# Optimization experiments

Hardware: AMD Instinct MI355X
Metric: run time of the kernel (lower is better)

The kernel has to match this reference:

```python
import jax, jax.numpy as jnp
import numpy as np

B, L, D, H = 8, 1024, 1024, 16
DPH = D // H  # 64


def setup_inputs() -> dict:
    key = jax.random.key(0)
    ks = jax.random.split(key, 12)
    s = 1.0 / np.sqrt(D)
    return {
        "key": jax.random.normal(ks[0], (B, L, D), jnp.float32),
        "value": jax.random.normal(ks[1], (B, L, D), jnp.float32),
        "query": jax.random.normal(ks[2], (B, L, D), jnp.float32),
        "attn_mask": jax.random.randint(ks[3], (B, L, L), 0, 2) > 0,
        "Wq": jax.random.normal(ks[4], (D, D), jnp.float32) * s,
        "bq": jnp.zeros((D,), jnp.float32),
        "Wk": jax.random.normal(ks[5], (D, D), jnp.float32) * s,
        "bk": jnp.zeros((D,), jnp.float32),
        "Wv": jax.random.normal(ks[6], (D, D), jnp.float32) * s,
        "bv": jnp.zeros((D,), jnp.float32),
        "Wo": jax.random.normal(ks[7], (D, D), jnp.float32) * s,
        "bo": jnp.zeros((D,), jnp.float32),
        "gamma": jnp.ones((D,), jnp.float32),
        "beta": jnp.zeros((D,), jnp.float32),
    }


def _layer_norm(x, gamma, beta, eps=1e-5):
    mu = jnp.mean(x, axis=-1, keepdims=True)
    var = jnp.var(x, axis=-1, keepdims=True)
    return (x - mu) * jax.lax.rsqrt(var + eps) * gamma + beta


def reference(key, value, query, attn_mask, Wq, bq, Wk, bk, Wv, bv, Wo, bo, gamma, beta):
    residual = query
    k = key @ Wk + bk      # [B, L, D]
    v = value @ Wv + bv
    q = query @ Wq + bq
    # faithful to torch: raw row-major view into [B*H, L, dph] (NOT standard head transpose)
    k = k.reshape(B * H, -1, DPH)
    v = v.reshape(B * H, -1, DPH)
    q = q.reshape(B * H, -1, DPH)
    # faithful to torch repeat: tile whole batch H times along dim 0
    mask = jnp.tile(attn_mask, (H, 1, 1))  # [B*H, L, L]
    scale = DPH ** (-0.5)
    scores = jnp.einsum('bqd,bkd->bqk', q, k) * scale
    scores = jnp.where(mask, jnp.float32(-1e9), scores)
    attention = jax.nn.softmax(scores, axis=2)
    context = jnp.einsum('bqk,bkd->bqd', attention, v)  # [B*H, L, dph]
    context = context.reshape(B, -1, D)
    output = context @ Wo + bo
    output = _layer_norm(residual + output, gamma, beta)
    return (output, attention)
```

## Files before the change

kernel.cpp:

```cpp
#include <hip/hip_runtime.h>

typedef __attribute__((ext_vector_type(8))) short short8;
typedef __attribute__((ext_vector_type(4))) float f32x4;

#define AS1C(p) ((const __attribute__((address_space(1))) void*)(p))
#define AS3(p)  ((__attribute__((address_space(3))) void*)(p))

__device__ __forceinline__ unsigned short f2bf(float f) {
  unsigned int u = __float_as_uint(f);
  return (unsigned short)((u + 0x7fffu + ((u >> 16) & 1u)) >> 16);
}

__device__ __forceinline__ void gload16(const void* g, void* l) {
  __builtin_amdgcn_global_load_lds(AS1C(g), AS3(l), 16, 0, 0);
}

#define EXP_C 0.18033688011112042f

__global__ __launch_bounds__(256) void conv3_bf16(const float* __restrict__ s0,
                                                  const float* __restrict__ s1,
                                                  const float* __restrict__ s2,
                                                  unsigned short* __restrict__ d0,
                                                  unsigned short* __restrict__ d1,
                                                  unsigned short* __restrict__ d2, int n4) {
  const float* in = (blockIdx.z == 0) ? s0 : (blockIdx.z == 1) ? s1 : s2;
  unsigned short* out = (blockIdx.z == 0) ? d0 : (blockIdx.z == 1) ? d1 : d2;
  int i = blockIdx.x * 256 + threadIdx.x;
  if (i >= n4) return;
  float4 v = ((const float4*)in)[i];
  ushort4 o;
  o.x = f2bf(v.x); o.y = f2bf(v.y); o.z = f2bf(v.z); o.w = f2bf(v.w);
  ((ushort4*)out)[i] = o;
}

__global__ __launch_bounds__(256) void prep_kernel(const float* __restrict__ W0,
                                                   const float* __restrict__ W1,
                                                   const float* __restrict__ W2,
                                                   const float* __restrict__ W3,
                                                   unsigned short* __restrict__ WtBase,
                                                   const int* __restrict__ m,
                                                   unsigned int* __restrict__ bitsT) {
  int bid = blockIdx.x;
  if (bid < 4096) {
    __shared__ float t[32][33];
    int z = bid >> 10;
    int rb = bid & 1023;
    int bx = (rb & 31) * 32, by = (rb >> 5) * 32;
    const float* W = (z == 0) ? W0 : (z == 1) ? W1 : (z == 2) ? W2 : W3;
    unsigned short* Wt = WtBase + (size_t)z * 1024 * 1024;
    int tx = threadIdx.x & 31, ty = threadIdx.x >> 5;
#pragma unroll
    for (int i = 0; i < 4; ++i) {
      int r = ty + i * 8;
      t[r][tx] = W[(size_t)(by + r) * 1024 + bx + tx];
    }
    __syncthreads();
#pragma unroll
    for (int i = 0; i < 4; ++i) {
      int r = ty + i * 8;
      Wt[(size_t)(bx + r) * 1024 + by + tx] = f2bf(t[tx][r]);
    }
  } else {
    int i = (bid - 4096) * 256 + threadIdx.x;
    unsigned long long bl = __ballot(m[i] != 0);
    if ((threadIdx.x & 63) == 0) {
      int b_ = i >> 20, q = (i >> 10) & 1023, k = i & 1023;
      int w = k >> 5;
      bitsT[b_ * 32768 + w * 1024 + q]       = (unsigned int)bl;
      bitsT[b_ * 32768 + (w + 1) * 1024 + q] = (unsigned int)(bl >> 32);
    }
  }
}

__global__ __launch_bounds__(256) void transpose_v(const unsigned short* __restrict__ v,
                                                   unsigned short* __restrict__ vt) {
  __shared__ unsigned short t[32][33];
  int b = blockIdx.z;
  int bx = blockIdx.x * 32;
  int by = blockIdx.y * 32;
  int tx = threadIdx.x & 31, ty = threadIdx.x >> 5;
#pragma unroll
  for (int i = 0; i < 4; ++i) {
    int r = ty + i * 8;
    t[r][tx] = v[(size_t)b * 65536 + (size_t)(by + r) * 64 + bx + tx];
  }
  __syncthreads();
#pragma unroll
  for (int i = 0; i < 4; ++i) {
    int r = ty + i * 8;
    vt[(size_t)b * 65536 + (size_t)(bx + r) * 1024 + by + tx] = t[tx][r];
  }
}

template <int MODE>
__device__ __forceinline__ void gemm_body(
    const unsigned short* __restrict__ A, const unsigned short* __restrict__ Bt,
    const float* __restrict__ bias, const float* __restrict__ res,
    unsigned short* __restrict__ Cb, float* __restrict__ Cf,
    unsigned short* lA, unsigned short* lB) {
  const int K = 1024, N = 1024;
  const int tid = threadIdx.x;
  const int wave = tid >> 6, lane = tid & 63;
  const int row_l = lane & 15, kg = lane >> 4;
  const int wg = blockIdx.y * 8 + blockIdx.x;
  const int idx = (wg & 7) * 64 + (wg >> 3);
  const int m0 = (idx >> 3) * 128, n0 = (idx & 7) * 128;
  const int wm = (wave >> 1) * 64, wn = (wave & 1) * 64;
  f32x4 acc[4][4] = {};

  for (int k0 = 0; k0 < K; k0 += 32) {
    __syncthreads();
#pragma unroll
    for (int it = 0; it < 2; ++it) {
      int c = wave * 64 + it * 256 + lane;
      int r = c >> 2, ch = c & 3;
      int sch = ch ^ (r & 3);
      gload16(A + (size_t)(m0 + r) * K + k0 + sch * 8, lA + (wave * 64 + it * 256) * 8);
      gload16(Bt + (size_t)(n0 + r) * K + k0 + sch * 8, lB + (wave * 64 + it * 256) * 8);
    }
    __syncthreads();
    short8 af[4], bfr[4];
#pragma unroll
    for (int t = 0; t < 4; ++t) {
      int ra = wm + t * 16 + row_l;
      af[t] = *(const short8*)(lA + ra * 32 + ((kg ^ (ra & 3)) << 3));
      int rb = wn + t * 16 + row_l;
      bfr[t] = *(const short8*)(lB + rb * 32 + ((kg ^ (rb & 3)) << 3));
    }
    __builtin_amdgcn_s_setprio(1);
#pragma unroll
    for (int mt = 0; mt < 4; ++mt)
#pragma unroll
      for (int nt = 0; nt < 4; ++nt)
        acc[mt][nt] = __builtin_amdgcn_mfma_f32_16x16x32_bf16(af[mt], bfr[nt], acc[mt][nt], 0, 0, 0);
    __builtin_amdgcn_s_setprio(0);
  }
#pragma unroll
  for (int mt = 0; mt < 4; ++mt)
#pragma unroll
    for (int nt = 0; nt < 4; ++nt)
#pragma unroll
      for (int r = 0; r < 4; ++r) {
        int grow = m0 + wm + mt * 16 + kg * 4 + r;
        int gcol = n0 + wn + nt * 16 + row_l;
        float v = acc[mt][nt][r] + bias[gcol];
        if (MODE == 0) {
          Cb[(size_t)grow * N + gcol] = f2bf(v);
        } else {
          v += res[(size_t)grow * N + gcol];
          Cf[(size_t)grow * N + gcol] = v;
        }
      }
}

__global__ __launch_bounds__(256) void gemm_qkv_kernel(
    const unsigned short* __restrict__ A0, const unsigned short* __restrict__ A1,
    const unsigned short* __restrict__ A2, const unsigned short* __restrict__ WtBase,
    const float* __restrict__ b0, const float* __restrict__ b1, const float* __restrict__ b2,
    unsigned short* __restrict__ C0, unsigned short* __restrict__ C1,
    unsigned short* __restrict__ C2) {
  __shared__ unsigned short lA[128 * 32];
  __shared__ unsigned short lB[128 * 32];
  int z = blockIdx.z;
  const unsigned short* A = (z == 0) ? A0 : (z == 1) ? A1 : A2;
  const float* bias = (z == 0) ? b0 : (z == 1) ? b1 : b2;
  unsigned short* C = (z == 0) ? C0 : (z == 1) ? C1 : C2;
  gemm_body<0>(A, WtBase + (size_t)z * 1024 * 1024, bias, nullptr, C, nullptr, lA, lB);
}

__global__ __launch_bounds__(256) void gemm_out_kernel(
    const unsigned short* __restrict__ A, const unsigned short* __restrict__ Bt,
    const float* __restrict__ bias, const float* __restrict__ res, float* __restrict__ Cf) {
  __shared__ unsigned short lA[128 * 32];
  __shared__ unsigned short lB[128 * 32];
  gemm_body<1>(A, Bt, bias, res, nullptr, Cf, lA, lB);
}

__global__ __launch_bounds__(256) void attn_kernel(
    const unsigned short* __restrict__ Q,
    const unsigned short* __restrict__ Km,
    const unsigned short* __restrict__ Vt,
    const unsigned int* __restrict__ mbitsT,
    float* __restrict__ attn,
    unsigned short* __restrict__ ctx) {
  __shared__ unsigned short lQ[64 * 64];
  __shared__ unsigned short lK[64 * 64];
  __shared__ unsigned short lV[64 * 64];
  const int tid = threadIdx.x, wave = tid >> 6, lane = tid & 63;
  const int row_l = lane & 15, kg = lane >> 4;
  const int wg = blockIdx.y * 16 + blockIdx.x;
  const int idx = (wg & 7) * 256 + (wg >> 3);
  const int batch = idx >> 4, qt = idx & 15;
  const int q0 = qt * 64;
  const unsigned short* Qb = Q + (size_t)batch * 65536;
  const unsigned short* Kb = Km + (size_t)batch * 65536;
  const unsigned short* Vb = Vt + (size_t)batch * 65536;
  const unsigned int* mT = mbitsT + (size_t)(batch & 7) * 32768;
  float* attb = attn + (size_t)batch * 1048576;
  const int q_loc = wave * 16 + row_l;
  const int q_lane = q0 + q_loc;

#define STAGE_K_TO(kt, dst)                                                           \
  {                                                                                   \
    _Pragma("unroll") for (int it = 0; it < 2; ++it) {                                \
      int c = wave * 64 + it * 256 + lane;                                            \
      int r_ = c >> 3, ch_ = c & 7, sch_ = ch_ ^ (r_ & 7);                            \
      gload16(Kb + (size_t)((kt) * 64 + r_) * 64 + sch_ * 8,                          \
              (dst) + (wave * 64 + it * 256) * 8);                                    \
    }                                                                                 \
  }
#define STAGE_V_TO(kt, dst)                                                           \
  {                                                                                   \
    _Pragma("unroll") for (int it = 0; it < 2; ++it) {                                \
      int c = wave * 64 + it * 256 + lane;                                            \
      int r_ = c >> 3, ch_ = c & 7, sch_ = ch_ ^ (r_ & 7);                            \
      gload16(Vb + (size_t)r_ * 1024 + (kt) * 64 + sch_ * 8,                          \
              (dst) + (wave * 64 + it * 256) * 8);                                    \
    }                                                                                 \
  }
#define WAIT_BAR0                                             \
  asm volatile("s_waitcnt vmcnt(0)" ::: "memory");            \
  __builtin_amdgcn_s_barrier();

#pragma unroll
  for (int it = 0; it < 2; ++it) {
    int c = wave * 64 + it * 256 + lane;
    int r = c >> 3, ch = c & 7;
    int sch = ch ^ (r & 7);
    gload16(Qb + (size_t)(q0 + r) * 64 + sch * 8, lQ + (wave * 64 + it * 256) * 8);
  }
  STAGE_K_TO(0, lK)
  WAIT_BAR0
  short8 qf[2];
#pragma unroll
  for (int kk = 0; kk < 2; ++kk)
    qf[kk] = *(const short8*)(lQ + q_loc * 64 + (((kk * 4 + kg) ^ (q_loc & 7)) << 3));

  float l_part = 0.f;

  auto pass1_step = [&](const unsigned short* kbuf, int kt) {
    unsigned int mw0 = mT[(kt * 2 + 0) * 1024 + q_lane];
    unsigned int mw1 = mT[(kt * 2 + 1) * 1024 + q_lane];
    f32x4 s[4];
    __builtin_amdgcn_s_setprio(1);
#pragma unroll
    for (int cf = 0; cf < 4; ++cf) {
      int rk = cf * 16 + row_l;
      f32x4 a = {0.f, 0.f, 0.f, 0.f};
#pragma unroll
      for (int kk = 0; kk < 2; ++kk) {
        short8 kf = *(const short8*)(kbuf + rk * 64 + (((kk * 4 + kg) ^ (rk & 7)) << 3));
        a = __builtin_amdgcn_mfma_f32_16x16x32_bf16(kf, qf[kk], a, 0, 0, 0);
      }
      s[cf] = a;
    }
    __builtin_amdgcn_s_setprio(0);
#pragma unroll
    for (int cf = 0; cf < 4; ++cf) {
      unsigned int w = (cf < 2) ? mw0 : mw1;
#pragma unroll
      for (int r = 0; r < 4; ++r) {
        int bit = (w >> ((cf & 1) * 16 + kg * 4 + r)) & 1;
        float e = __builtin_exp2f(s[cf][r] * EXP_C);
        l_part += bit ? 0.f : e;
      }
    }
  };
  for (int kt2 = 0; kt2 < 16; kt2 += 2) {
    STAGE_K_TO(kt2 + 1, lV)
    pass1_step(lK, kt2);
    WAIT_BAR0
    if (kt2 + 2 < 16) STAGE_K_TO(kt2 + 2, lK)
    pass1_step(lV, kt2 + 1);
    WAIT_BAR0
  }
  float se = l_part;
  se += __shfl_xor(se, 16);
  se += __shfl_xor(se, 32);
  const float il = 1.f / se;

  f32x4 cacc[4] = {};
  unsigned short* lP = lQ;

  for (int kt = 0; kt < 16; ++kt) {
    __syncthreads();
    STAGE_K_TO(kt, lK)
    STAGE_V_TO(kt, lV)
    WAIT_BAR0
    unsigned int mw0 = mT[(kt * 2 + 0) * 1024 + q_lane];
    unsigned int mw1 = mT[(kt * 2 + 1) * 1024 + q_lane];
    f32x4 s[4];
    __builtin_amdgcn_s_setprio(1);
#pragma unroll
    for (int cf = 0; cf < 4; ++cf) {
      int rk = cf * 16 + row_l;
      f32x4 a = {0.f, 0.f, 0.f, 0.f};
#pragma unroll
      for (int kk = 0; kk < 2; ++kk) {
        short8 kf = *(const short8*)(lK + rk * 64 + (((kk * 4 + kg) ^ (rk & 7)) << 3));
        a = __builtin_amdgcn_mfma_f32_16x16x32_bf16(kf, qf[kk], a, 0, 0, 0);
      }
      s[cf] = a;
    }
    __builtin_amdgcn_s_setprio(0);
#pragma unroll
    for (int cf = 0; cf < 4; ++cf) {
      unsigned int w = (cf < 2) ? mw0 : mw1;
      f32x4 o;
      unsigned short pb[4];
#pragma unroll
      for (int r = 0; r < 4; ++r) {
        int bit = (w >> ((cf & 1) * 16 + kg * 4 + r)) & 1;
        float p = bit ? 0.f : __builtin_exp2f(s[cf][r] * EXP_C) * il;
        o[r] = p;
        pb[r] = f2bf(p);
      }
      int swc = (cf * 2 + (kg >> 1)) ^ (q_loc & 7);
      *(uint2*)((char*)lP + q_loc * 128 + swc * 16 + (kg & 1) * 8) = *(const uint2*)pb;
      __builtin_nontemporal_store(
          o, (f32x4*)(attb + (size_t)q_lane * 1024 + kt * 64 + cf * 16 + kg * 4));
    }
    __builtin_amdgcn_s_setprio(1);
#pragma unroll
    for (int kk = 0; kk < 2; ++kk) {
      short8 pa = *(const short8*)(lP + q_loc * 64 + (((kk * 4 + kg) ^ (q_loc & 7)) << 3));
#pragma unroll
      for (int df = 0; df < 4; ++df) {
        int rv = df * 16 + row_l;
        short8 vb = *(const short8*)(lV + rv * 64 + (((kk * 4 + kg) ^ (rv & 7)) << 3));
        cacc[df] = __builtin_amdgcn_mfma_f32_16x16x32_bf16(pa, vb, cacc[df], 0, 0, 0);
      }
    }
    __builtin_amdgcn_s_setprio(0);
  }
#pragma unroll
  for (int df = 0; df < 4; ++df)
#pragma unroll
    for (int r = 0; r < 4; ++r) {
      int grow = q0 + wave * 16 + kg * 4 + r;
      int gcol = df * 16 + row_l;
      ctx[(size_t)batch * 65536 + (size_t)grow * 64 + gcol] = f2bf(cacc[df][r]);
    }
#undef STAGE_K_TO
#undef STAGE_V_TO
#undef WAIT_BAR0
}

__global__ __launch_bounds__(256) void layernorm_kernel(float* __restrict__ io,
                                                        const float* __restrict__ gamma,
                                                        const float* __restrict__ beta) {
  int wave = threadIdx.x >> 6, lane = threadIdx.x & 63;
  size_t row = (size_t)blockIdx.x * 4 + wave;
  float* p = io + row * 1024;
  float4 v[4];
  float s = 0.f, ss = 0.f;
#pragma unroll
  for (int i = 0; i < 4; ++i) {
    v[i] = ((const float4*)p)[lane + i * 64];
    s += v[i].x + v[i].y + v[i].z + v[i].w;
    ss += v[i].x * v[i].x + v[i].y * v[i].y + v[i].z * v[i].z + v[i].w * v[i].w;
  }
#pragma unroll
  for (int m = 1; m < 64; m <<= 1) { s += __shfl_xor(s, m); ss += __shfl_xor(ss, m); }
  float mu = s * (1.f / 1024.f);
  float var = ss * (1.f / 1024.f) - mu * mu;
  float rinv = rsqrtf(var + 1e-5f);
#pragma unroll
  for (int i = 0; i < 4; ++i) {
    int idx = lane + i * 64;
    float4 g = ((const float4*)gamma)[idx];
    float4 b = ((const float4*)beta)[idx];
    float4 o;
    o.x = (v[i].x - mu) * rinv * g.x + b.x;
    o.y = (v[i].y - mu) * rinv * g.y + b.y;
    o.z = (v[i].z - mu) * rinv * g.z + b.z;
    o.w = (v[i].w - mu) * rinv * g.w + b.w;
    ((float4*)p)[idx] = o;
  }
}

extern "C" void kernel_launch(void* const* d_in, const int* in_sizes, int n_in,
                              void* d_out, int out_size, void* d_ws, size_t ws_size,
                              hipStream_t stream) {
  const float* key   = (const float*)d_in[0];
  const float* value = (const float*)d_in[1];
  const float* query = (const float*)d_in[2];
  const int* amask   = (const int*)d_in[3];
  const float* Wq = (const float*)d_in[4];
  const float* bq = (const float*)d_in[5];
  const float* Wk = (const float*)d_in[6];
  const float* bk = (const float*)d_in[7];
  const float* Wv = (const float*)d_in[8];
  const float* bv = (const float*)d_in[9];
  const float* Wo = (const float*)d_in[10];
  const float* bo = (const float*)d_in[11];
  const float* gamma = (const float*)d_in[12];
  const float* beta  = (const float*)d_in[13];

  char* ws = (char*)d_ws;
  const size_t MB = 1024 * 1024;
  float* out_f = (float*)d_out;
  float* attn_f = (float*)d_out + (size_t)8388608;
  const int n4 = 8388608 / 4;
  dim3 gemm_grid(8, 64);
  dim3 gemm_grid3(8, 64, 3);
  dim3 attn_grid(16, 128);

  const bool big_ws = ws_size >= 106 * MB;
  if (big_ws) {
    unsigned short* A0 = (unsigned short*)(ws + 0);
    unsigned short* A1 = (unsigned short*)(ws + 16 * MB);
    unsigned short* A2 = (unsigned short*)(ws + 32 * MB);
    unsigned short* B1 = (unsigned short*)(ws + 48 * MB);
    unsigned short* B2 = (unsigned short*)(ws + 64 * MB);
    unsigned short* B3 = (unsigned short*)(ws + 80 * MB);
    unsigned short* Wts = (unsigned short*)(ws + 96 * MB);
    unsigned int* mbitsT = (unsigned int*)(ws + 104 * MB);

    prep_kernel<<<36864, 256, 0, stream>>>(Wq, Wk, Wv, Wo, Wts, amask, mbitsT);
    conv3_bf16<<<dim3(8192, 1, 3), 256, 0, stream>>>(query, key, value, A0, A1, A2, n4);
    gemm_qkv_kernel<<<gemm_grid3, 256, 0, stream>>>(A0, A1, A2, Wts, bq, bk, bv, B1, B2, B3);
    transpose_v<<<dim3(2, 32, 128), 256, 0, stream>>>(B3, A1);
    attn_kernel<<<attn_grid, 256, 0, stream>>>(B1, B2, A1, mbitsT, attn_f, A2);
    gemm_out_kernel<<<gemm_grid, 256, 0, stream>>>(A2, Wts + 3 * MB, bo, query, out_f);
    layernorm_kernel<<<2048, 256, 0, stream>>>(out_f, gamma, beta);
  } else {
    unsigned short* B0 = (unsigned short*)(ws + 0);
    unsigned short* B1 = (unsigned short*)(ws + 16 * MB);
    unsigned short* B2 = (unsigned short*)(ws + 32 * MB);
    unsigned short* B3 = (unsigned short*)(ws + 48 * MB);
    unsigned short* Wts = (unsigned short*)(ws + 64 * MB);
    unsigned int* mbitsT = (unsigned int*)(ws + 72 * MB);

    prep_kernel<<<36864, 256, 0, stream>>>(Wq, Wk, Wv, Wo, Wts, amask, mbitsT);
    conv3_bf16<<<dim3(8192, 1, 1), 256, 0, stream>>>(query, query, query, B0, B0, B0, n4);
    gemm_qkv_kernel<<<gemm_grid, 256, 0, stream>>>(B0, B0, B0, Wts, bq, bq, bq, B1, B1, B1);
    conv3_bf16<<<dim3(8192, 1, 1), 256, 0, stream>>>(key, key, key, B0, B0, B0, n4);
    gemm_qkv_kernel<<<gemm_grid, 256, 0, stream>>>(B0, B0, B0, Wts + 1 * MB, bk, bk, bk, B2, B2, B2);
    conv3_bf16<<<dim3(8192, 1, 1), 256, 0, stream>>>(value, value, value, B0, B0, B0, n4);
    gemm_qkv_kernel<<<gemm_grid, 256, 0, stream>>>(B0, B0, B0, Wts + 2 * MB, bv, bv, bv, B3, B3, B3);
    transpose_v<<<dim3(2, 32, 128), 256, 0, stream>>>(B3, B0);
    attn_kernel<<<attn_grid, 256, 0, stream>>>(B1, B2, B0, mbitsT, attn_f, B3);
    gemm_out_kernel<<<gemm_grid, 256, 0, stream>>>(B3, Wts + 3 * MB, bo, query, out_f);
    layernorm_kernel<<<2048, 256, 0, stream>>>(out_f, gamma, beta);
  }
}
```

Before: 344.0 us.

## Double GEMM K-tile to 64 and fold input bf16 conversion into prep kernel

The GEMM mainloop now stages a 64-wide K slice per iteration instead of 32, using an 8-way XOR swizzle, and runs two MFMA sub-steps per barrier pair. This halves the number of synchronisation rounds and global-to-LDS load phases. LDS use per block doubles to 32 KB, which may lower occupancy. Separately, the fp32-to-bf16 conversion of query/key/value is merged into prep_kernel as extra blocks, saving one kernel launch on the large-workspace path.

After: 321.6 us. 6.5% less time.

```diff
diff --git a/kernel.cpp b/kernel.cpp
--- a/kernel.cpp
+++ b/kernel.cpp
@@ -16,22 +16,6 @@
 }
 
 #define EXP_C 0.18033688011112042f
-
-__global__ __launch_bounds__(256) void conv3_bf16(const float* __restrict__ s0,
-                                                  const float* __restrict__ s1,
-                                                  const float* __restrict__ s2,
-                                                  unsigned short* __restrict__ d0,
-                                                  unsigned short* __restrict__ d1,
-                                                  unsigned short* __restrict__ d2, int n4) {
-  const float* in = (blockIdx.z == 0) ? s0 : (blockIdx.z == 1) ? s1 : s2;
-  unsigned short* out = (blockIdx.z == 0) ? d0 : (blockIdx.z == 1) ? d1 : d2;
-  int i = blockIdx.x * 256 + threadIdx.x;
-  if (i >= n4) return;
-  float4 v = ((const float4*)in)[i];
-  ushort4 o;
-  o.x = f2bf(v.x); o.y = f2bf(v.y); o.z = f2bf(v.z); o.w = f2bf(v.w);
-  ((ushort4*)out)[i] = o;
-}
 
 __global__ __launch_bounds__(256) void prep_kernel(const float* __restrict__ W0,
                                                    const float* __restrict__ W1,
@@ -39,7 +23,13 @@
                                                    const float* __restrict__ W3,
                                                    unsigned short* __restrict__ WtBase,
                                                    const int* __restrict__ m,
-                                                   unsigned int* __restrict__ bitsT) {
+                                                   unsigned int* __restrict__ bitsT,
+                                                   const float* __restrict__ s0,
+                                                   const float* __restrict__ s1,
+                                                   const float* __restrict__ s2,
+                                                   unsigned short* __restrict__ d0,
+                                                   unsigned short* __restrict__ d1,
+                                                   unsigned short* __restrict__ d2) {
   int bid = blockIdx.x;
   if (bid < 4096) {
     __shared__ float t[32][33];
@@ -60,7 +50,7 @@
       int r = ty + i * 8;
       Wt[(size_t)(bx + r) * 1024 + by + tx] = f2bf(t[tx][r]);
     }
-  } else {
+  } else if (bid < 36864) {
     int i = (bid - 4096) * 256 + threadIdx.x;
     unsigned long long bl = __ballot(m[i] != 0);
     if ((threadIdx.x & 63) == 0) {
@@ -69,7 +59,27 @@
       bitsT[b_ * 32768 + w * 1024 + q]       = (unsigned int)bl;
       bitsT[b_ * 32768 + (w + 1) * 1024 + q] = (unsigned int)(bl >> 32);
     }
-  }
+  } else {
+    int cb = bid - 36864;
+    int z = cb >> 13;
+    const float* in = (z == 0) ? s0 : (z == 1) ? s1 : s2;
+    unsigned short* out = (z == 0) ? d0 : (z == 1) ? d1 : d2;
+    int i = (cb & 8191) * 256 + threadIdx.x;
+    float4 v = ((const float4*)in)[i];
+    ushort4 o;
+    o.x = f2bf(v.x); o.y = f2bf(v.y); o.z = f2bf(v.z); o.w = f2bf(v.w);
+    ((ushort4*)out)[i] = o;
+  }
+}
+
+__global__ __launch_bounds__(256) void conv_bf16(const float* __restrict__ in,
+                                                 unsigned short* __restrict__ out, int n4) {
+  int i = blockIdx.x * 256 + threadIdx.x;
+  if (i >= n4) return;
+  float4 v = ((const float4*)in)[i];
+  ushort4 o;
+  o.x = f2bf(v.x); o.y = f2bf(v.y); o.z = f2bf(v.z); o.w = f2bf(v.w);
+  ((ushort4*)out)[i] = o;
 }
 
 __global__ __launch_bounds__(256) void transpose_v(const unsigned short* __restrict__ v,
@@ -108,32 +118,35 @@
   const int wm = (wave >> 1) * 64, wn = (wave & 1) * 64;
   f32x4 acc[4][4] = {};
 
-  for (int k0 = 0; k0 < K; k0 += 32) {
+  for (int k0 = 0; k0 < K; k0 += 64) {
     __syncthreads();
 #pragma unroll
-    for (int it = 0; it < 2; ++it) {
+    for (int it = 0; it < 4; ++it) {
       int c = wave * 64 + it * 256 + lane;
-      int r = c >> 2, ch = c & 3;
-      int sch = ch ^ (r & 3);
+      int r = c >> 3, ch = c & 7;
+      int sch = ch ^ (r & 7);
       gload16(A + (size_t)(m0 + r) * K + k0 + sch * 8, lA + (wave * 64 + it * 256) * 8);
       gload16(Bt + (size_t)(n0 + r) * K + k0 + sch * 8, lB + (wave * 64 + it * 256) * 8);
     }
     __syncthreads();
-    short8 af[4], bfr[4];
-#pragma unroll
-    for (int t = 0; t < 4; ++t) {
-      int ra = wm + t * 16 + row_l;
-      af[t] = *(const short8*)(lA + ra * 32 + ((kg ^ (ra & 3)) << 3));
-      int rb = wn + t * 16 + row_l;
-      bfr[t] = *(const short8*)(lB + rb * 32 + ((kg ^ (rb & 3)) << 3));
-    }
-    __builtin_amdgcn_s_setprio(1);
-#pragma unroll
-    for (int mt = 0; mt < 4; ++mt)
-#pragma unroll
-      for (int nt = 0; nt < 4; ++nt)
-        acc[mt][nt] = __builtin_amdgcn_mfma_f32_16x16x32_bf16(af[mt], bfr[nt], acc[mt][nt], 0, 0, 0);
-    __builtin_amdgcn_s_setprio(0);
+#pragma unroll
+    for (int kk = 0; kk < 2; ++kk) {
+      short8 af[4], bfr[4];
+#pragma unroll
+      for (int t = 0; t < 4; ++t) {
+        int ra = wm + t * 16 + row_l;
+        af[t] = *(const short8*)(lA + ra * 64 + (((kk * 4 + kg) ^ (ra & 7)) << 3));
+        int rb = wn + t * 16 + row_l;
+        bfr[t] = *(const short8*)(lB + rb * 64 + (((kk * 4 + kg) ^ (rb & 7)) << 3));
+      }
+      __builtin_amdgcn_s_setprio(1);
+#pragma unroll
+      for (int mt = 0; mt < 4; ++mt)
+#pragma unroll
+        for (int nt = 0; nt < 4; ++nt)
+          acc[mt][nt] = __builtin_amdgcn_mfma_f32_16x16x32_bf16(af[mt], bfr[nt], acc[mt][nt], 0, 0, 0);
+      __builtin_amdgcn_s_setprio(0);
+    }
   }
 #pragma unroll
   for (int mt = 0; mt < 4; ++mt)
@@ -159,8 +172,8 @@
     const float* __restrict__ b0, const float* __restrict__ b1, const float* __restrict__ b2,
     unsigned short* __restrict__ C0, unsigned short* __restrict__ C1,
     unsigned short* __restrict__ C2) {
-  __shared__ unsigned short lA[128 * 32];
-  __shared__ unsigned short lB[128 * 32];
+  __shared__ unsigned short lA[128 * 64];
+  __shared__ unsigned short lB[128 * 64];
   int z = blockIdx.z;
   const unsigned short* A = (z == 0) ? A0 : (z == 1) ? A1 : A2;
   const float* bias = (z == 0) ? b0 : (z == 1) ? b1 : b2;
@@ -171,8 +184,8 @@
 __global__ __launch_bounds__(256) void gemm_out_kernel(
     const unsigned short* __restrict__ A, const unsigned short* __restrict__ Bt,
     const float* __restrict__ bias, const float* __restrict__ res, float* __restrict__ Cf) {
-  __shared__ unsigned short lA[128 * 32];
-  __shared__ unsigned short lB[128 * 32];
+  __shared__ unsigned short lA[128 * 64];
+  __shared__ unsigned short lB[128 * 64];
   gemm_body<1>(A, Bt, bias, res, nullptr, Cf, lA, lB);
 }
 
@@ -417,8 +430,8 @@
     unsigned short* Wts = (unsigned short*)(ws + 96 * MB);
     unsigned int* mbitsT = (unsigned int*)(ws + 104 * MB);
 
-    prep_kernel<<<36864, 256, 0, stream>>>(Wq, Wk, Wv, Wo, Wts, amask, mbitsT);
-    conv3_bf16<<<dim3(8192, 1, 3), 256, 0, stream>>>(query, key, value, A0, A1, A2, n4);
+    prep_kernel<<<61440, 256, 0, stream>>>(Wq, Wk, Wv, Wo, Wts, amask, mbitsT,
+                                           query, key, value, A0, A1, A2);
     gemm_qkv_kernel<<<gemm_grid3, 256, 0, stream>>>(A0, A1, A2, Wts, bq, bk, bv, B1, B2, B3);
     transpose_v<<<dim3(2, 32, 128), 256, 0, stream>>>(B3, A1);
     attn_kernel<<<attn_grid, 256, 0, stream>>>(B1, B2, A1, mbitsT, attn_f, A2);
@@ -432,12 +445,13 @@
     unsigned short* Wts = (unsigned short*)(ws + 64 * MB);
     unsigned int* mbitsT = (unsigned int*)(ws + 72 * MB);
 
-    prep_kernel<<<36864, 256, 0, stream>>>(Wq, Wk, Wv, Wo, Wts, amask, mbitsT);
-    conv3_bf16<<<dim3(8192, 1, 1), 256, 0, stream>>>(query, query, query, B0, B0, B0, n4);
+    prep_kernel<<<36864, 256, 0, stream>>>(Wq, Wk, Wv, Wo, Wts, amask, mbitsT,
+                                           query, key, value, B0, B0, B0);
+    conv_bf16<<<8192, 256, 0, stream>>>(query, B0, n4);
     gemm_qkv_kernel<<<gemm_grid, 256, 0, stream>>>(B0, B0, B0, Wts, bq, bq, bq, B1, B1, B1);
-    conv3_bf16<<<dim3(8192, 1, 1), 256, 0, stream>>>(key, key, key, B0, B0, B0, n4);
+    conv_bf16<<<8192, 256, 0, stream>>>(key, B0, n4);
     gemm_qkv_kernel<<<gemm_grid, 256, 0, stream>>>(B0, B0, B0, Wts + 1 * MB, bk, bk, bk, B2, B2, B2);
-    conv3_bf16<<<dim3(8192, 1, 1), 256, 0, stream>>>(value, value, value, B0, B0, B0, n4);
+    conv_bf16<<<8192, 256, 0, stream>>>(value, B0, n4);
     gemm_qkv_kernel<<<gemm_grid, 256, 0, stream>>>(B0, B0, B0, Wts + 2 * MB, bv, bv, bv, B3, B3, B3);
     transpose_v<<<dim3(2, 32, 128), 256, 0, stream>>>(B3, B0);
     attn_kernel<<<attn_grid, 256, 0, stream>>>(B1, B2, B0, mbitsT, attn_f, B3);
```
